# Kernel optimization log

Measured on AMD Instinct MI355X. Metric: run time of the kernel, lower is better.

The kernel has to match this reference:

```python
import jax, jax.numpy as jnp
import numpy as np

B, DIM, SIZE, NF = 16, 192, 48, 8
C2 = DIM // 2 + 1            # channel-rfft length (97)
HID = int(0.25 * DIM)        # reweight Mlp hidden (48)
FS = SIZE // 2 + 1           # spatial rfft width (25)
EPS = 1e-5


def setup_inputs() -> dict:
    key = jax.random.key(0)
    ks = jax.random.split(key, 12)
    n = lambda i, shape, s=0.02: jax.random.normal(ks[i], shape, jnp.float32) * s
    return {
        "r": jax.random.normal(ks[0], (B, DIM, SIZE, SIZE), jnp.float32),
        "t": jax.random.normal(ks[1], (B, DIM, SIZE, SIZE), jnp.float32),
        # BatchNorm2d (eval mode, running stats mean=0, var=1): [bn_r; bn_t]
        "bn_g": jnp.ones((2, DIM), jnp.float32),
        "bn_b": jnp.zeros((2, DIM), jnp.float32),
        # conv_r / conv_t 1x1 (with bias)
        "crt_w": n(2, (2, DIM, DIM)),
        "crt_b": jnp.zeros((2, DIM), jnp.float32),
        # StarReLU scale/bias: [act_r, act_t, mlp.act]
        "star_s": jnp.ones((3,), jnp.float32),
        "star_b": jnp.zeros((3,), jnp.float32),
        # reweight Mlp (bias=False)
        "fc1_w": n(3, (HID, DIM)),
        "fc2_w": n(4, (NF * DIM, HID)),
        # complex_weights [size, filter_size, num_filters, 2]
        "cw": n(5, (SIZE, FS, NF, 2)),
        # channel-spectrum enhance nets [rc_a, rc_p, tc_a, tc_p], each conv1x1->lrelu->conv1x1
        "enh_w1": n(6, (4, C2, C2)), "enh_b1": jnp.zeros((4, C2), jnp.float32),
        "enh_w2": n(7, (4, C2, C2)), "enh_b2": jnp.zeros((4, C2), jnp.float32),
        # conv_phase_r / conv_phase_t, each conv1x1->lrelu->conv1x1
        "ph_w1": n(8, (2, DIM, DIM)), "ph_b1": jnp.zeros((2, DIM), jnp.float32),
        "ph_w2": n(9, (2, DIM, DIM)), "ph_b2": jnp.zeros((2, DIM), jnp.float32),
        # DwconvFFN: BN (eval) + depthwise 3x3 (no bias)
        "dwbn_g": jnp.ones((DIM,), jnp.float32),
        "dwbn_b": jnp.zeros((DIM,), jnp.float32),
        "dw_w": n(10, (DIM, 1, 3, 3)),
    }


def _leaky(x):
    return jnp.where(x >= 0, x, 0.1 * x)


def _c1(x, w, b):  # 1x1 conv, NCHW
    return jnp.einsum('bchw,oc->bohw', x, w) + b[None, :, None, None]


def _net(x, w1, b1, w2, b2):  # conv1x1 -> LeakyReLU(0.1) -> conv1x1
    return _c1(_leaky(_c1(x, w1, b1)), w2, b2)


def _star(x, s, b):  # StarReLU: s * relu(x)^2 + b
    return s * jnp.square(jnp.maximum(x, 0.0)) + b


def _bn(x, g, b):  # eval-mode BN with running mean=0, var=1
    return x * (g / jnp.sqrt(1.0 + EPS))[None, :, None, None] + b[None, :, None, None]


def _forward(r, t, bn_g, bn_b, crt_w, crt_b, star_s, star_b, fc1_w, fc2_w, cw,
             enh_w1, enh_b1, enh_w2, enh_b2, ph_w1, ph_b1, ph_w2, ph_b2,
             dwbn_g, dwbn_b, dw_w):
    Bsz, D, H, W = r.shape
    res_r, res_t = r, t
    r = _bn(r, bn_g[0], bn_b[0])
    t = _bn(t, bn_g[1], bn_b[1])
    x = r + t
    # routeing: Mlp(mean over HW) -> [B, NF, D] softmax over filters
    h = _star(x.mean((2, 3)) @ fc1_w.T, star_s[2], star_b[2])
    route = jax.nn.softmax((h @ fc2_w.T).reshape(Bsz, NF, D), axis=1)
    r = _star(_c1(r, crt_w[0], crt_b[0]), star_s[0], star_b[0])
    t = _star(_c1(t, crt_w[1], crt_b[1]), star_s[1], star_b[1])

    def branch(u, ia, ip, iph):
        u_fft = jnp.fft.rfft2(u, axes=(2, 3), norm='ortho')   # [B,D,H,FS]
        a = jnp.abs(u_fft)
        p = jnp.angle(u_fft)
        cf = jnp.fft.rfft(a, axis=1, norm='ortho')            # channel rfft -> [B,C2,H,FS]
        ca, cp = jnp.abs(cf), jnp.angle(cf)
        caE = _net(ca, enh_w1[ia], enh_b1[ia], enh_w2[ia], enh_b2[ia])
        cpE = _net(cp, enh_w1[ip], enh_b1[ip], enh_w2[ip], enh_b2[ip])
        comp = caE * jnp.cos(cpE) + 1j * (caE * jnp.sin(cpE))
        c = jnp.fft.irfft(comp, n=D, axis=1, norm='ortho')    # back to [B,D,H,FS]
        sc = c * a
        pE = _net(p, ph_w1[iph], ph_b1[iph], ph_w2[iph], ph_b2[iph])
        return sc * jnp.cos(pE) + 1j * (sc * jnp.sin(pE))

    rt_s = branch(r, 0, 1, 0) + branch(t, 2, 3, 1)            # [B,D,H,FS] complex
    weight = cw[..., 0] + 1j * cw[..., 1]                     # [H,FS,NF]
    weights = jnp.einsum('bfc,hwf->bchw', route.astype(jnp.complex64), weight)
    rt = jnp.fft.irfft2(rt_s * weights, s=(H, W), axes=(2, 3), norm='ortho')
    out_1 = rt + res_r + res_t
    y = _bn(out_1, dwbn_g, dwbn_b)
    y = jax.lax.conv_general_dilated(
        y, dw_w, (1, 1), 'SAME',
        dimension_numbers=('NCHW', 'OIHW', 'NCHW'), feature_group_count=D)
    return y + out_1


def reference(r, t, bn_g, bn_b, crt_w, crt_b, star_s, star_b, fc1_w, fc2_w, cw,
              enh_w1, enh_b1, enh_w2, enh_b2, ph_w1, ph_b1, ph_w2, ph_b2,
              dwbn_g, dwbn_b, dw_w):
    return _forward(r, t, bn_g, bn_b, crt_w, crt_b, star_s, star_b, fc1_w, fc2_w, cw,
                    enh_w1, enh_b1, enh_w2, enh_b2, ph_w1, ph_b1, ph_w2, ph_b2,
                    dwbn_g, dwbn_b, dw_w)
```

## Files before the change

### kernel.cpp

```cpp
#include <hip/hip_runtime.h>
#include <math.h>

constexpr int B_   = 16;
constexpr int D_   = 192;
constexpr int S_   = 48;
constexpr int NF_  = 8;
constexpr int C2_  = 97;
constexpr int HID_ = 48;
constexpr int FS_  = 25;
constexpr int HW_  = S_ * S_;
constexpr int HWF_ = S_ * FS_;
constexpr int CIN2_ = 2 * C2_;
constexpr float EPS_ = 1e-5f;
constexpr double PI_D = 3.14159265358979323846;

__global__ __launch_bounds__(192) void k_prep(const float* __restrict__ crt_w,
                                              const float* __restrict__ crt_b,
                                              const float* __restrict__ bn_g,
                                              const float* __restrict__ bn_b,
                                              float* __restrict__ Weff,
                                              float* __restrict__ beff)
{
    int io = blockIdx.x;
    int c  = threadIdx.x;
    int i  = io / D_;
    float s  = bn_g[i * D_ + c] * rsqrtf(1.f + EPS_);
    float bb = bn_b[i * D_ + c];
    float w  = crt_w[(size_t)io * D_ + c];
    Weff[(size_t)io * D_ + c] = w * s;
    __shared__ float red[D_];
    red[c] = w * bb;
    __syncthreads();
    if (c == 0) {
        float acc = 0.f;
        for (int j = 0; j < D_; ++j) acc += red[j];
        int o = io % D_;
        beff[io] = crt_b[i * D_ + o] + acc;
    }
}

__global__ __launch_bounds__(192) void k_twidf(float* __restrict__ TWF)
{
    int k = blockIdx.x;
    int d = threadIdx.x;
    double ang = 2.0 * PI_D * (double)(k * d) / (double)D_;
    float nrm = rsqrtf((float)D_);
    TWF[k * D_ + d]              = (float)cos(ang) * nrm;
    TWF[C2_ * D_ + k * D_ + d]   = (float)(-sin(ang)) * nrm;
}

__global__ __launch_bounds__(256) void k_twidi(float* __restrict__ TWI)
{
    int d = blockIdx.x;
    int k = threadIdx.x;
    if (k >= CIN2_) return;
    float nrm = rsqrtf((float)D_);
    int j = (k < C2_) ? k : k - C2_;
    double ang = 2.0 * PI_D * (double)(j * d) / (double)D_;
    float v;
    if (k < C2_) {
        if (j == 0)       v = nrm;
        else if (j == 96) v = (d & 1) ? -nrm : nrm;
        else              v = 2.f * (float)cos(ang) * nrm;
    } else {
        if (j == 0 || j == 96) v = 0.f;
        else                   v = -2.f * (float)sin(ang) * nrm;
    }
    TWI[d * CIN2_ + k] = v;
}

__global__ __launch_bounds__(256) void k_mean(const float* __restrict__ r,
                                              const float* __restrict__ t,
                                              const float* __restrict__ bn_g,
                                              const float* __restrict__ bn_b,
                                              float* __restrict__ xm)
{
    int bd = blockIdx.x;
    int d  = bd % D_;
    float sr = bn_g[d]      * rsqrtf(1.f + EPS_);
    float st = bn_g[D_ + d] * rsqrtf(1.f + EPS_);
    const float* rp = r + (size_t)bd * HW_;
    const float* tp = t + (size_t)bd * HW_;
    float acc = 0.f;
    for (int i = threadIdx.x; i < HW_; i += 256) acc += rp[i] * sr + tp[i] * st;
    __shared__ float red[256];
    red[threadIdx.x] = acc;
    __syncthreads();
    for (int off = 128; off > 0; off >>= 1) {
        if (threadIdx.x < off) red[threadIdx.x] += red[threadIdx.x + off];
        __syncthreads();
    }
    if (threadIdx.x == 0)
        xm[bd] = red[0] * (1.f / HW_) + bn_b[d] + bn_b[D_ + d];
}

__global__ __launch_bounds__(192) void k_route(const float* __restrict__ xm,
                                               const float* __restrict__ fc1,
                                               const float* __restrict__ fc2,
                                               const float* __restrict__ star_s,
                                               const float* __restrict__ star_b,
                                               float* __restrict__ route)
{
    int b = blockIdx.x;
    int tid = threadIdx.x;
    __shared__ float x[D_];
    __shared__ float h[HID_];
    x[tid] = xm[b * D_ + tid];
    __syncthreads();
    if (tid < HID_) {
        float a = 0.f;
        const float* wp = fc1 + (size_t)tid * D_;
        for (int c = 0; c < D_; ++c) a += x[c] * wp[c];
        float rl = fmaxf(a, 0.f);
        h[tid] = star_s[2] * rl * rl + star_b[2];
    }
    __syncthreads();
    float lg[NF_];
    for (int f = 0; f < NF_; ++f) {
        const float* wp = fc2 + ((size_t)f * D_ + tid) * HID_;
        float a = 0.f;
        for (int j = 0; j < HID_; ++j) a += h[j] * wp[j];
        lg[f] = a;
    }
    float m = lg[0];
    for (int f = 1; f < NF_; ++f) m = fmaxf(m, lg[f]);
    float ssum = 0.f;
    for (int f = 0; f < NF_; ++f) { lg[f] = expf(lg[f] - m); ssum += lg[f]; }
    float inv = 1.f / ssum;
    for (int f = 0; f < NF_; ++f)
        route[((size_t)b * NF_ + f) * D_ + tid] = lg[f] * inv;
}

__global__ __launch_bounds__(256) void k_gemm(const float* __restrict__ in,
                                              const float* __restrict__ W,
                                              const float* __restrict__ bias,
                                              float* __restrict__ outp,
                                              int Cin, int Cout, int HWl, int NB, int act,
                                              const float* __restrict__ ssp,
                                              const float* __restrict__ sbp, int sidx,
                                              long instr, long wstr, long bstr, long ostr,
                                              const float* __restrict__ scp,
                                              float* __restrict__ rre,
                                              float* __restrict__ rim, int addf)
{
    const int z = blockIdx.z;
    in   += (long)z * instr;
    W    += (long)z * wstr;
    if (bias) bias += (long)z * bstr;
    outp += (long)z * ostr;

    const int n0 = blockIdx.x * 128;
    const int o0 = blockIdx.y * 64;
    const int tid = threadIdx.x;
    const int tx = tid & 15;
    const int ty = tid >> 4;
    __shared__ float As[16][72];
    __shared__ float Bs[16][136];
    float acc[4][8] = {};
    const int Ntot = NB * HWl;

    const int akk = tid & 15, aoo0 = tid >> 4;
    const int nn = tid & 127, kb = tid >> 7;
    const int n = n0 + nn;
    const bool nok = n < Ntot;
    int bidx = 0, hw = 0;
    if (nok) { bidx = n / HWl; hw = n % HWl; }
    const float* bp = in + (size_t)bidx * Cin * HWl + hw;

    for (int k0 = 0; k0 < Cin; k0 += 16) {
        #pragma unroll
        for (int j = 0; j < 4; ++j) {
            int oo = aoo0 + 16 * j;
            int o  = o0 + oo;
            int k  = k0 + akk;
            As[akk][oo] = (o < Cout && k < Cin) ? W[(size_t)o * Cin + k] : 0.f;
        }
        #pragma unroll
        for (int j = 0; j < 8; ++j) {
            int kk = kb * 8 + j;
            int k  = k0 + kk;
            Bs[kk][nn] = (nok && k < Cin) ? bp[(size_t)k * HWl] : 0.f;
        }
        __syncthreads();
        #pragma unroll
        for (int kk = 0; kk < 16; ++kk) {
            float4 av = *reinterpret_cast<const float4*>(&As[kk][ty * 4]);
            float4 b0 = *reinterpret_cast<const float4*>(&Bs[kk][tx * 8]);
            float4 b1 = *reinterpret_cast<const float4*>(&Bs[kk][tx * 8 + 4]);
            float a4[4] = {av.x, av.y, av.z, av.w};
            float b8[8] = {b0.x, b0.y, b0.z, b0.w, b1.x, b1.y, b1.z, b1.w};
            #pragma unroll
            for (int i = 0; i < 4; ++i)
                #pragma unroll
                for (int j = 0; j < 8; ++j)
                    acc[i][j] += a4[i] * b8[j];
        }
        __syncthreads();
    }

    float ss = 0.f, sb = 0.f;
    if (act == 2) { ss = ssp[sidx]; sb = sbp[sidx]; }
    #pragma unroll
    for (int i = 0; i < 4; ++i) {
        int o = o0 + ty * 4 + i;
        if (o >= Cout) continue;
        float bs = bias ? bias[o] : 0.f;
        #pragma unroll
        for (int j = 0; j < 8; ++j) {
            int nj = n0 + tx * 8 + j;
            if (nj >= Ntot) continue;
            float v = acc[i][j] + bs;
            int bb = nj / HWl, hh = nj % HWl;
            size_t oi = ((size_t)bb * Cout + o) * HWl + hh;
            if (act == 3) {
                float s = scp[oi];
                float sn, cs; sincosf(v, &sn, &cs);
                float re = s * cs, im = s * sn;
                if (addf) { rre[oi] += re; rim[oi] += im; }
                else      { rre[oi]  = re; rim[oi]  = im; }
            } else if (act == 4) {
                outp[oi] = v * scp[oi];
            } else {
                if (act == 1)      v = v >= 0.f ? v : 0.1f * v;
                else if (act == 2) { float rl = fmaxf(v, 0.f); v = ss * rl * rl + sb; }
                outp[oi] = v;
            }
        }
    }
}

__global__ __launch_bounds__(256) void k_rfft2(const float* __restrict__ u,
                                               float* __restrict__ A,
                                               float* __restrict__ P)
{
    int bd = blockIdx.x;
    __shared__ float tu[HW_];
    __shared__ float rre[HWF_], rim[HWF_];
    __shared__ float tc[S_], ts[S_];
    int t = threadIdx.x;
    if (t < S_) { double ang = -2.0 * PI_D * (double)t / (double)S_; tc[t] = (float)cos(ang); ts[t] = (float)sin(ang); }
    for (int i = t; i < HW_; i += 256) tu[i] = u[(size_t)bd * HW_ + i];
    __syncthreads();
    for (int i = t; i < HWF_; i += 256) {
        int h = i / FS_, k = i % FS_;
        float ar = 0.f, ai = 0.f;
        int m = 0;
        for (int w = 0; w < S_; ++w) {
            float v = tu[h * S_ + w];
            ar += v * tc[m]; ai += v * ts[m];
            m += k; if (m >= S_) m -= S_;
        }
        rre[i] = ar; rim[i] = ai;
    }
    __syncthreads();
    for (int i = t; i < HWF_; i += 256) {
        int kh = i / FS_, w = i % FS_;
        float ar = 0.f, ai = 0.f;
        int m = 0;
        for (int h = 0; h < S_; ++h) {
            float xr = rre[h * FS_ + w], xi = rim[h * FS_ + w];
            float c = tc[m], s = ts[m];
            ar += xr * c - xi * s;
            ai += xr * s + xi * c;
            m += kh; if (m >= S_) m -= S_;
        }
        ar *= (1.f / 48.f); ai *= (1.f / 48.f);
        A[(size_t)bd * HWF_ + i] = sqrtf(ar * ar + ai * ai);
        P[(size_t)bd * HWF_ + i] = atan2f(ai, ar);
    }
}

__global__ __launch_bounds__(256) void k_absang(float* __restrict__ CF, long slot)
{
    for (long i = (long)blockIdx.x * 256 + threadIdx.x; i < slot; i += (long)gridDim.x * 256) {
        float re = CF[i], im = CF[slot + i];
        CF[i]        = sqrtf(re * re + im * im);
        CF[slot + i] = atan2f(im, re);
    }
}

__global__ __launch_bounds__(256) void k_buildri(const float* __restrict__ CF,
                                                 float* __restrict__ RI, long slot)
{
    const long row = (long)C2_ * HWF_;
    const long brow = (long)CIN2_ * HWF_;
    for (long i = (long)blockIdx.x * 256 + threadIdx.x; i < slot; i += (long)gridDim.x * 256) {
        long b = i / row;
        long r = i % row;
        float amp = CF[i], ph = CF[slot + i];
        float sn, cs; sincosf(ph, &sn, &cs);
        RI[b * brow + r]                    = amp * cs;
        RI[b * brow + (long)C2_ * HWF_ + r] = amp * sn;
    }
}

__global__ __launch_bounds__(256) void k_final(const float* __restrict__ rre,
                                               const float* __restrict__ rim,
                                               const float* __restrict__ route,
                                               const float* __restrict__ cw,
                                               const float* __restrict__ rin,
                                               const float* __restrict__ tin,
                                               float* __restrict__ out1)
{
    int bd = blockIdx.x;
    int b = bd / D_, d = bd % D_;
    __shared__ float sRe[HWF_], sIm[HWF_];
    __shared__ float cRe[HWF_], cIm[HWF_];
    __shared__ float tc[S_], ts[S_];
    __shared__ float rt[NF_];
    int t = threadIdx.x;
    if (t < S_) { double ang = 2.0 * PI_D * (double)t / (double)S_; tc[t] = (float)cos(ang); ts[t] = (float)sin(ang); }
    if (t < NF_) rt[t] = route[((size_t)b * NF_ + t) * D_ + d];
    __syncthreads();
    for (int i = t; i < HWF_; i += 256) {
        const float* cwp = cw + (size_t)i * NF_ * 2;
        float wr = 0.f, wi = 0.f;
        #pragma unroll
        for (int f = 0; f < NF_; ++f) { wr += rt[f] * cwp[2 * f]; wi += rt[f] * cwp[2 * f + 1]; }
        float xr = rre[(size_t)bd * HWF_ + i], xi = rim[(size_t)bd * HWF_ + i];
        sRe[i] = xr * wr - xi * wi;
        sIm[i] = xr * wi + xi * wr;
    }
    __syncthreads();
    for (int i = t; i < HWF_; i += 256) {
        int hp = i / FS_, w = i % FS_;
        float ar = 0.f, ai = 0.f;
        int m = 0;
        for (int h = 0; h < S_; ++h) {
            float xr = sRe[h * FS_ + w], xi = sIm[h * FS_ + w];
            ar += xr * tc[m] - xi * ts[m];
            ai += xr * ts[m] + xi * tc[m];
            m += hp; if (m >= S_) m -= S_;
        }
        cRe[i] = ar; cIm[i] = ai;
    }
    __syncthreads();
    for (int i = t; i < HW_; i += 256) {
        int hp = i / S_, n = i % S_;
        float acc = cRe[hp * FS_] + ((n & 1) ? -1.f : 1.f) * cRe[hp * FS_ + FS_ - 1];
        float s2 = 0.f;
        int m = n;
        for (int k = 1; k < FS_ - 1; ++k) {
            s2 += cRe[hp * FS_ + k] * tc[m] - cIm[hp * FS_ + k] * ts[m];
            m += n; if (m >= S_) m -= S_;
        }
        float v = (acc + 2.f * s2) * (1.f / 48.f);
        size_t o = (size_t)bd * HW_ + i;
        out1[o] = v + rin[o] + tin[o];
    }
}

__global__ __launch_bounds__(256) void k_dw(const float* __restrict__ out1,
                                            const float* __restrict__ g,
                                            const float* __restrict__ bbn,
                                            const float* __restrict__ wdw,
                                            float* __restrict__ outp)
{
    int bd = blockIdx.x;
    int d = bd % D_;
    __shared__ float tile[HW_];
    int t = threadIdx.x;
    for (int i = t; i < HW_; i += 256) tile[i] = out1[(size_t)bd * HW_ + i];
    float sc = g[d] * rsqrtf(1.f + EPS_);
    float bb = bbn[d];
    float w9[9];
    #pragma unroll
    for (int q = 0; q < 9; ++q) w9[q] = wdw[d * 9 + q];
    __syncthreads();
    for (int i = t; i < HW_; i += 256) {
        int y = i / S_, x = i % S_;
        float acc = 0.f;
        #pragma unroll
        for (int ki = 0; ki < 3; ++ki) {
            int yy = y + ki - 1;
            if (yy < 0 || yy >= S_) continue;
            #pragma unroll
            for (int kj = 0; kj < 3; ++kj) {
                int xx = x + kj - 1;
                if (xx < 0 || xx >= S_) continue;
                acc += w9[ki * 3 + kj] * (tile[yy * S_ + xx] * sc + bb);
            }
        }
        outp[(size_t)bd * HW_ + i] = acc + tile[i];
    }
}

extern "C" void kernel_launch(void* const* d_in, const int* in_sizes, int n_in,
                              void* d_out, int out_size, void* d_ws, size_t ws_size,
                              hipStream_t stream)
{
    (void)in_sizes; (void)n_in; (void)out_size; (void)ws_size;
    const float* r      = (const float*)d_in[0];
    const float* t      = (const float*)d_in[1];
    const float* bn_g   = (const float*)d_in[2];
    const float* bn_b   = (const float*)d_in[3];
    const float* crt_w  = (const float*)d_in[4];
    const float* crt_b  = (const float*)d_in[5];
    const float* star_s = (const float*)d_in[6];
    const float* star_b = (const float*)d_in[7];
    const float* fc1_w  = (const float*)d_in[8];
    const float* fc2_w  = (const float*)d_in[9];
    const float* cw     = (const float*)d_in[10];
    const float* enh_w1 = (const float*)d_in[11];
    const float* enh_b1 = (const float*)d_in[12];
    const float* enh_w2 = (const float*)d_in[13];
    const float* enh_b2 = (const float*)d_in[14];
    const float* ph_w1  = (const float*)d_in[15];
    const float* ph_b1  = (const float*)d_in[16];
    const float* ph_w2  = (const float*)d_in[17];
    const float* ph_b2  = (const float*)d_in[18];
    const float* dwbn_g = (const float*)d_in[19];
    const float* dwbn_b = (const float*)d_in[20];
    const float* dw_w   = (const float*)d_in[21];
    float* out = (float*)d_out;

    const long NDHWF = (long)B_ * D_ * HWF_;
    const long SLOTC = (long)B_ * C2_ * HWF_;

    float* ws = (float*)d_ws;
    size_t off = 0;
    float* UACT = ws + off; off += (size_t)B_ * D_ * HW_;
    float* A_   = ws + off; off += NDHWF;
    float* P_   = ws + off; off += NDHWF;
    float* RRE  = ws + off; off += NDHWF;
    float* RIM  = ws + off; off += NDHWF;
    float* CA2  = ws + off; off += 2 * SLOTC;
    float* XM   = ws + off; off += B_ * D_;
    float* ROUTE= ws + off; off += B_ * NF_ * D_;
    float* WEFF = ws + off; off += 2 * D_ * D_;
    float* BEFF = ws + off; off += 2 * D_;
    float* TWF  = ws + off; off += 2 * C2_ * D_;
    float* TWI  = ws + off; off += (size_t)D_ * CIN2_;
    float* CH   = UACT;
    float* RI   = UACT;
    float* HT   = UACT;

    k_prep<<<2 * D_, D_, 0, stream>>>(crt_w, crt_b, bn_g, bn_b, WEFF, BEFF);
    k_twidf<<<C2_, D_, 0, stream>>>(TWF);
    k_twidi<<<D_, 256, 0, stream>>>(TWI);
    k_mean<<<B_ * D_, 256, 0, stream>>>(r, t, bn_g, bn_b, XM);
    k_route<<<B_, 192, 0, stream>>>(XM, fc1_w, fc2_w, star_s, star_b, ROUTE);

    for (int br = 0; br < 2; ++br) {
        const float* u_in = (br == 0) ? r : t;
        const int ia = (br == 0) ? 0 : 2;

        k_gemm<<<dim3(288, 3, 1), 256, 0, stream>>>(u_in, WEFF + (size_t)br * D_ * D_, BEFF + br * D_,
            UACT, D_, D_, HW_, B_, 2, star_s, star_b, br, 0, 0, 0, 0, nullptr, nullptr, nullptr, 0);
        k_rfft2<<<B_ * D_, 256, 0, stream>>>(UACT, A_, P_);
        k_gemm<<<dim3(150, 2, 2), 256, 0, stream>>>(A_, TWF, nullptr,
            CA2, D_, C2_, HWF_, B_, 0, nullptr, nullptr, 0,
            0, (long)C2_ * D_, 0, SLOTC, nullptr, nullptr, nullptr, 0);
        k_absang<<<1024, 256, 0, stream>>>(CA2, SLOTC);
        k_gemm<<<dim3(150, 2, 2), 256, 0, stream>>>(CA2, enh_w1 + (size_t)ia * C2_ * C2_, enh_b1 + ia * C2_,
            CH, C2_, C2_, HWF_, B_, 1, nullptr, nullptr, 0,
            SLOTC, (long)C2_ * C2_, C2_, SLOTC, nullptr, nullptr, nullptr, 0);
        k_gemm<<<dim3(150, 2, 2), 256, 0, stream>>>(CH, enh_w2 + (size_t)ia * C2_ * C2_, enh_b2 + ia * C2_,
            CA2, C2_, C2_, HWF_, B_, 0, nullptr, nullptr, 0,
            SLOTC, (long)C2_ * C2_, C2_, SLOTC, nullptr, nullptr, nullptr, 0);
        k_buildri<<<1024, 256, 0, stream>>>(CA2, RI, SLOTC);
        k_gemm<<<dim3(150, 3, 1), 256, 0, stream>>>(RI, TWI, nullptr,
            A_, CIN2_, D_, HWF_, B_, 4, nullptr, nullptr, 0,
            0, 0, 0, 0, A_, nullptr, nullptr, 0);
        k_gemm<<<dim3(150, 3, 1), 256, 0, stream>>>(P_, ph_w1 + (size_t)br * D_ * D_, ph_b1 + br * D_,
            HT, D_, D_, HWF_, B_, 1, nullptr, nullptr, 0, 0, 0, 0, 0, nullptr, nullptr, nullptr, 0);
        k_gemm<<<dim3(150, 3, 1), 256, 0, stream>>>(HT, ph_w2 + (size_t)br * D_ * D_, ph_b2 + br * D_,
            P_, D_, D_, HWF_, B_, 3, nullptr, nullptr, 0, 0, 0, 0, 0, A_, RRE, RIM, br);
    }

    k_final<<<B_ * D_, 256, 0, stream>>>(RRE, RIM, ROUTE, cw, r, t, UACT);
    k_dw<<<B_ * D_, 256, 0, stream>>>(UACT, dwbn_g, dwbn_b, dw_w, out);
}
```

Before: 1.443 ms.

## Factor 48-point column DFT into 4x12 Cooley-Tukey stages in rfft2 and final kernels

Replaces the direct 48-point DFT along the H axis in k_rfft2 and k_final with a two-stage mixed-radix decomposition: twelve 12-point DFTs over stride-4 subsequences, then 4-point combines with twiddles. This cuts the per-output multiply-add count from 48 to 16 complex terms and fully unrolls the inner loops. In exchange it adds extra shared-memory buffers (yre/yim), which lowers occupancy, and an extra __syncthreads per kernel.

```diff
diff --git a/kernel.cpp b/kernel.cpp
--- a/kernel.cpp
+++ b/kernel.cpp
@@ -236,6 +236,7 @@
     int bd = blockIdx.x;
     __shared__ float tu[HW_];
     __shared__ float rre[HWF_], rim[HWF_];
+    __shared__ float yre[HWF_], yim[HWF_];
     __shared__ float tc[S_], ts[S_];
     int t = threadIdx.x;
     if (t < S_) { double ang = -2.0 * PI_D * (double)t / (double)S_; tc[t] = (float)cos(ang); ts[t] = (float)sin(ang); }
@@ -254,15 +255,32 @@
     }
     __syncthreads();
     for (int i = t; i < HWF_; i += 256) {
-        int kh = i / FS_, w = i % FS_;
+        int r = i / 300, j = (i / FS_) % 12, w = i % FS_;
         float ar = 0.f, ai = 0.f;
-        int m = 0;
-        for (int h = 0; h < S_; ++h) {
-            float xr = rre[h * FS_ + w], xi = rim[h * FS_ + w];
-            float c = tc[m], s = ts[m];
+        int mj = 0;
+        #pragma unroll
+        for (int m = 0; m < 12; ++m) {
+            int hh = 4 * m + r;
+            float xr = rre[hh * FS_ + w], xi = rim[hh * FS_ + w];
+            float c = tc[4 * mj], s = ts[4 * mj];
             ar += xr * c - xi * s;
             ai += xr * s + xi * c;
-            m += kh; if (m >= S_) m -= S_;
+            mj += j; if (mj >= 12) mj -= 12;
+        }
+        yre[i] = ar; yim[i] = ai;
+    }
+    __syncthreads();
+    for (int i = t; i < HWF_; i += 256) {
+        int kh = i / FS_, w = i % FS_, j = kh % 12;
+        float ar = 0.f, ai = 0.f;
+        int rk = 0;
+        #pragma unroll
+        for (int r = 0; r < 4; ++r) {
+            float xr = yre[(r * 12 + j) * FS_ + w], xi = yim[(r * 12 + j) * FS_ + w];
+            float c = tc[rk], s = ts[rk];
+            ar += xr * c - xi * s;
+            ai += xr * s + xi * c;
+            rk += kh; if (rk >= S_) rk -= S_;
         }
         ar *= (1.f / 48.f); ai *= (1.f / 48.f);
         A[(size_t)bd * HWF_ + i] = sqrtf(ar * ar + ai * ai);
@@ -305,6 +323,7 @@
     int bd = blockIdx.x;
     int b = bd / D_, d = bd % D_;
     __shared__ float sRe[HWF_], sIm[HWF_];
+    __shared__ float yre[HWF_], yim[HWF_];
     __shared__ float cRe[HWF_], cIm[HWF_];
     __shared__ float tc[S_], ts[S_];
     __shared__ float rt[NF_];
@@ -323,14 +342,32 @@
     }
     __syncthreads();
     for (int i = t; i < HWF_; i += 256) {
-        int hp = i / FS_, w = i % FS_;
+        int r = i / 300, j = (i / FS_) % 12, w = i % FS_;
         float ar = 0.f, ai = 0.f;
-        int m = 0;
-        for (int h = 0; h < S_; ++h) {
-            float xr = sRe[h * FS_ + w], xi = sIm[h * FS_ + w];
-            ar += xr * tc[m] - xi * ts[m];
-            ai += xr * ts[m] + xi * tc[m];
-            m += hp; if (m >= S_) m -= S_;
+        int mj = 0;
+        #pragma unroll
+        for (int m = 0; m < 12; ++m) {
+            int hh = 4 * m + r;
+            float xr = sRe[hh * FS_ + w], xi = sIm[hh * FS_ + w];
+            float c = tc[4 * mj], s = ts[4 * mj];
+            ar += xr * c - xi * s;
+            ai += xr * s + xi * c;
+            mj += j; if (mj >= 12) mj -= 12;
+        }
+        yre[i] = ar; yim[i] = ai;
+    }
+    __syncthreads();
+    for (int i = t; i < HWF_; i += 256) {
+        int hp = i / FS_, w = i % FS_, j = hp % 12;
+        float ar = 0.f, ai = 0.f;
+        int rk = 0;
+        #pragma unroll
+        for (int r = 0; r < 4; ++r) {
+            float xr = yre[(r * 12 + j) * FS_ + w], xi = yim[(r * 12 + j) * FS_ + w];
+            float c = tc[rk], s = ts[rk];
+            ar += xr * c - xi * s;
+            ai += xr * s + xi * c;
+            rk += hp; if (rk >= S_) rk -= S_;
         }
         cRe[i] = ar; cIm[i] = ai;
     }
```

Result: faster. 1.347 ms (-6.6%).
